# Optimization experiments

Measured on AMD Instinct MI355X. Metric: run time of the kernel, lower is better.

The kernel has to match this reference:

```python
import jax, jax.numpy as jnp
import numpy as np
import math

B, S, D, H, R, DFF = 4, 1024, 1024, 16, 64, 4096

def _layernorm(x, g, b, eps=1e-5):
    m = jnp.mean(x, axis=-1, keepdims=True)
    v = jnp.var(x, axis=-1, keepdims=True)
    return (x - m) / jnp.sqrt(v + eps) * g + b

def setup_inputs() -> dict:
    key = jax.random.key(0)
    ks = jax.random.split(key, 12)
    sc = 0.02
    return {
        "src": jax.random.normal(ks[0], (B, S, D), jnp.float32),
        "in_proj_w": jax.random.normal(ks[1], (3 * D, D), jnp.float32) * sc,
        "in_proj_b": jnp.zeros((3 * D,), jnp.float32),
        "out_proj_w": jax.random.normal(ks[2], (D, D), jnp.float32) * sc,
        "out_proj_b": jnp.zeros((D,), jnp.float32),
        "Qp_w": jax.random.normal(ks[3], (R, D), jnp.float32) * sc,
        "Qp_b": jnp.zeros((R,), jnp.float32),
        "Kp_w": jax.random.normal(ks[4], (R, D), jnp.float32) * sc,
        "Kp_b": jnp.zeros((R,), jnp.float32),
        "Vp_w": jax.random.normal(ks[5], (D, D), jnp.float32) * sc,
        "Vp_b": jnp.zeros((D,), jnp.float32),
        "lam": jnp.float32(0.5),
        "ff1_w": jax.random.normal(ks[6], (DFF, D), jnp.float32) * sc,
        "ff1_b": jnp.zeros((DFF,), jnp.float32),
        "ff2_w": jax.random.normal(ks[7], (D, DFF), jnp.float32) * sc,
        "ff2_b": jnp.zeros((D,), jnp.float32),
        "ln1_g": jnp.ones((D,), jnp.float32),
        "ln1_b": jnp.zeros((D,), jnp.float32),
        "ln2_g": jnp.ones((D,), jnp.float32),
        "ln2_b": jnp.zeros((D,), jnp.float32),
    }

def reference(src, in_proj_w, in_proj_b, out_proj_w, out_proj_b,
              Qp_w, Qp_b, Kp_w, Kp_b, Vp_w, Vp_b, lam,
              ff1_w, ff1_b, ff2_w, ff2_b, ln1_g, ln1_b, ln2_g, ln2_b):
    b, s, d = src.shape
    dh = d // H
    # ---- dense multi-head attention (torch nn.MultiheadAttention, eval) ----
    qkv = src @ in_proj_w.T + in_proj_b            # [B,S,3D]
    q, k, v = jnp.split(qkv, 3, axis=-1)
    q = q.reshape(b, s, H, dh).transpose(0, 2, 1, 3)  # [B,H,S,dh]
    k = k.reshape(b, s, H, dh).transpose(0, 2, 1, 3)
    v = v.reshape(b, s, H, dh).transpose(0, 2, 1, 3)
    scores = jnp.einsum('bhqd,bhkd->bhqk', q, k) / math.sqrt(dh)
    attn = jax.nn.softmax(scores, axis=-1)
    ctx = jnp.einsum('bhqk,bhkd->bhqd', attn, v)
    ctx = ctx.transpose(0, 2, 1, 3).reshape(b, s, d)
    dense_output = ctx @ out_proj_w.T + out_proj_b
    # ---- low-rank top-k sparse attention ----
    Q = src @ Qp_w.T + Qp_b                        # [B,S,R]
    K = src @ Kp_w.T + Kp_b
    V = src @ Vp_w.T + Vp_b                        # [B,S,D]
    QK = jnp.einsum('bqr,bkr->bqk', Q, K) / math.sqrt(R)
    aw = jax.nn.softmax(QK, axis=-1)               # [B,S,S]
    kk = max(1, int(s * 0.2))
    topv, topi = jax.lax.top_k(aw, kk)             # [B,S,kk]
    bi = jnp.arange(b)[:, None, None]
    si = jnp.arange(s)[None, :, None]
    sparse_attn = jnp.zeros_like(aw).at[bi, si, topi].set(topv)
    sparse_attn = sparse_attn / (jnp.sum(sparse_attn, axis=-1, keepdims=True) + 1e-9)
    sparse_output = jnp.einsum('bqk,bkd->bqd', sparse_attn, V)
    # ---- fuse, residual, norm, FFN ----
    sig = jax.nn.sigmoid(lam)
    fused = sig * dense_output + (1.0 - sig) * sparse_output
    x = _layernorm(src + fused, ln1_g, ln1_b)
    ff = jax.nn.relu(x @ ff1_w.T + ff1_b) @ ff2_w.T + ff2_b
    return _layernorm(x + ff, ln2_g, ln2_b)
```

## Files before the change

kernel.cpp:

```cpp
#include <hip/hip_runtime.h>
#include <hip/hip_bf16.h>
#include <math.h>

typedef __hip_bfloat16 bf16;
typedef __attribute__((ext_vector_type(8))) short short8;
typedef __attribute__((ext_vector_type(4))) float f32x4;

#define NB 4
#define NS 1024
#define ND 1024
#define NH 16
#define NDH 64
#define NR 64
#define NDFF 4096
#define NM (NB*NS)
#define NTOPK 204

static __device__ __forceinline__ float b2f(bf16 x) { return __bfloat162float(x); }
static __device__ __forceinline__ bf16  f2b(float x) { return __float2bfloat16(x); }
static __device__ __forceinline__ unsigned short bfbits(float x) {
  bf16 h = __float2bfloat16(x);
  return *reinterpret_cast<unsigned short*>(&h);
}

static __device__ __forceinline__ void gload_lds16(const void* g, void* l) {
  __builtin_amdgcn_global_load_lds(
      (const __attribute__((address_space(1))) void*)g,
      (__attribute__((address_space(3))) void*)l, 16, 0, 0);
}

template<int N> static __device__ __forceinline__ void vm_wait() {
  if constexpr (N == 0)       asm volatile("s_waitcnt vmcnt(0)" ::: "memory");
  else if constexpr (N == 2)  asm volatile("s_waitcnt vmcnt(2)" ::: "memory");
  else if constexpr (N == 4)  asm volatile("s_waitcnt vmcnt(4)" ::: "memory");
  else if constexpr (N == 6)  asm volatile("s_waitcnt vmcnt(6)" ::: "memory");
  else if constexpr (N == 8)  asm volatile("s_waitcnt vmcnt(8)" ::: "memory");
  else if constexpr (N == 12) asm volatile("s_waitcnt vmcnt(12)" ::: "memory");
  else static_assert(N == 0, "unsupported vmcnt");
}
static __device__ __forceinline__ void bar() {
  asm volatile("s_barrier" ::: "memory");
}

static __device__ __forceinline__ void ld8(const bf16* p, float* d) {
  const uint4 u = *(const uint4*)p;
  d[0] = __uint_as_float((u.x & 0xffffu) << 16);
  d[1] = __uint_as_float(u.x & 0xffff0000u);
  d[2] = __uint_as_float((u.y & 0xffffu) << 16);
  d[3] = __uint_as_float(u.y & 0xffff0000u);
  d[4] = __uint_as_float((u.z & 0xffffu) << 16);
  d[5] = __uint_as_float(u.z & 0xffff0000u);
  d[6] = __uint_as_float((u.w & 0xffffu) << 16);
  d[7] = __uint_as_float(u.w & 0xffff0000u);
}

static __device__ __forceinline__ float block_sum_256(float v, float* rbuf, int tid) {
  rbuf[tid] = v;
  __syncthreads();
  #pragma unroll
  for (int st = 128; st > 0; st >>= 1) {
    if (tid < st) rbuf[tid] += rbuf[tid + st];
    __syncthreads();
  }
  const float r = rbuf[0];
  __syncthreads();
  return r;
}

struct CastArgs {
  const float* in[6];
  bf16* out[6];
  unsigned end[6];
};
__global__ __launch_bounds__(256) void cast6_kernel(CastArgs a) {
  const unsigned b = blockIdx.x;
  int r = 0; unsigned base = 0;
  #pragma unroll
  for (int k = 0; k < 5; ++k)
    if (b >= a.end[k]) { r = k + 1; base = a.end[k]; }
  const float* in = a.in[r];
  bf16* out = a.out[r];
  const unsigned i = ((b - base) * 256 + threadIdx.x) * 4;
  const float4 v = *(const float4*)(in + i);
  uint2 o;
  o.x = (unsigned)bfbits(v.x) | ((unsigned)bfbits(v.y) << 16);
  o.y = (unsigned)bfbits(v.z) | ((unsigned)bfbits(v.w) << 16);
  *(uint2*)(out + i) = o;
}

__global__ __launch_bounds__(256) void pack_qk_kernel(
    const float* __restrict__ Qw, const float* __restrict__ Kw,
    const float* __restrict__ Qb, const float* __restrict__ Kb,
    bf16* __restrict__ w, float* __restrict__ bias) {
  const int r = blockIdx.x;
  const float* srcw = (r < 64) ? (Qw + (size_t)r * ND) : (Kw + (size_t)(r - 64) * ND);
  for (int i = threadIdx.x; i < ND; i += 256) w[(size_t)r * ND + i] = f2b(srcw[i]);
  if (r == 0)
    for (int i = threadIdx.x; i < 128; i += 256)
      bias[i] = (i < 64) ? Qb[i] : Kb[i - 64];
}

template<int BM, int BN, int BK, int BIAS, int RELU, int OUTF32>
__global__ __launch_bounds__(256) void mfma_gemm(
    const bf16* __restrict__ A, const bf16* __restrict__ W,
    const float* __restrict__ bias, void* __restrict__ C,
    int K, int lda, int ldb, int ldc,
    long long aHi, long long aLo, long long bHi, long long bLo,
    long long cHi, long long cLo, float scale)
{
  constexpr int WTM = BM / 2;
  constexpr int WTN = BN / 2;
  constexpr int AM = WTM / 16;
  constexpr int AN = WTN / 16;
  constexpr int KK = BK / 32;
  constexpr int SLOTS = BK / 8;
  constexpr int RPC = 512 / BK;
  constexpr int LPW = (BM * BK) / 2048 + (BN * BK) / 2048;
  __shared__ short As[2][BM * BK];
  __shared__ short Bs[2][BN * BK];
  const int tid  = threadIdx.x;
  const int lane = tid & 63;
  const int w    = tid >> 6;
  const int z    = blockIdx.z;
  const long long aOff = (long long)(z >> 4) * aHi + (long long)(z & 15) * aLo;
  const long long bOff = (long long)(z >> 4) * bHi + (long long)(z & 15) * bLo;
  const long long cOff = (long long)(z >> 4) * cHi + (long long)(z & 15) * cLo;

  int bx = blockIdx.x, by = blockIdx.y;
  if ((gridDim.x & 7) == 0) {
    const unsigned lin = blockIdx.y * gridDim.x + blockIdx.x;
    const unsigned Wd = gridDim.x >> 3;
    const unsigned xcd = lin & 7, i = lin >> 3;
    bx = (int)(xcd * Wd + (i % Wd));
    by = (int)(i / Wd);
  }
  const int m0 = by * BM;
  const int n0 = bx * BN;
  const int wr = w >> 1, wc = w & 1;
  const int lm = lane & 15, quad = lane >> 4;

  f32x4 acc[AM][AN];
  #pragma unroll
  for (int i = 0; i < AM; ++i)
    #pragma unroll
    for (int j = 0; j < AN; ++j) acc[i][j] = (f32x4){0.f, 0.f, 0.f, 0.f};

  const int slot = lane & (SLOTS - 1);
  const int sr   = lane / SLOTS;
  const int swz  = (BK == 32) ? ((sr >> 1) & 3) : (sr & 7);
  const int scol = (slot ^ swz) << 3;
  const int xv   = (BK == 32) ? ((lm >> 1) & 3) : (lm & 7);
  const bf16* Ab = A + aOff;
  const bf16* Bb = W + bOff;

  auto stage = [&](int buf, int k0) {
    #pragma unroll
    for (int t = 0; t < (BM * BK) / 2048; ++t) {
      const int row = w * (BM / 4) + t * RPC;
      gload_lds16(Ab + (long long)(m0 + row + sr) * lda + k0 + scol, &As[buf][row * BK]);
    }
    #pragma unroll
    for (int t = 0; t < (BN * BK) / 2048; ++t) {
      const int row = w * (BN / 4) + t * RPC;
      gload_lds16(Bb + (long long)(n0 + row + sr) * ldb + k0 + scol, &Bs[buf][row * BK]);
    }
  };
  auto compute = [&](int buf) {
    #pragma unroll
    for (int kk = 0; kk < KK; ++kk) {
      const int cb = ((kk * 4 + quad) ^ xv) << 3;
      short8 af[AM], bfr[AN];
      #pragma unroll
      for (int i = 0; i < AM; ++i)
        af[i] = *(const short8*)&As[buf][(wr * WTM + i * 16 + lm) * BK + cb];
      #pragma unroll
      for (int j = 0; j < AN; ++j)
        bfr[j] = *(const short8*)&Bs[buf][(wc * WTN + j * 16 + lm) * BK + cb];
      #pragma unroll
      for (int i = 0; i < AM; ++i)
        #pragma unroll
        for (int j = 0; j < AN; ++j)
          acc[i][j] = __builtin_amdgcn_mfma_f32_16x16x32_bf16(af[i], bfr[j], acc[i][j], 0, 0, 0);
    }
  };

  stage(0, 0);
  int cur = 0;
  for (int k0 = BK; k0 < K; k0 += BK) {
    stage(cur ^ 1, k0);
    vm_wait<LPW>();
    bar();
    compute(cur);
    bar();
    cur ^= 1;
  }
  vm_wait<0>();
  bar();
  compute(cur);

  #pragma unroll
  for (int i = 0; i < AM; ++i) {
    #pragma unroll
    for (int j = 0; j < AN; ++j) {
      const int n = n0 + wc * WTN + j * 16 + lm;
      const float bj = BIAS ? bias[n] : 0.f;
      #pragma unroll
      for (int rr = 0; rr < 4; ++rr) {
        const int m = m0 + wr * WTM + i * 16 + quad * 4 + rr;
        float v = acc[i][j][rr] * scale + bj;
        if (RELU) v = fmaxf(v, 0.f);
        const long long co = cOff + (long long)m * ldc + n;
        if (OUTF32) ((float*)C)[co] = v;
        else        ((bf16*)C)[co] = f2b(v);
      }
    }
  }
}

__global__ __launch_bounds__(256) void attn_kernel(
    const bf16* __restrict__ qkv,
    const bf16* __restrict__ Vt,
    bf16* __restrict__ ctx)
{
  __shared__ short smem[2][2][64 * 64];
  const int tid = threadIdx.x, lane = tid & 63, w = tid >> 6;
  const int lm = lane & 15, quad = lane >> 4;
  const int z = blockIdx.y, b = z >> 4, h = z & 15;
  const int q0 = blockIdx.x * 128;
  const bf16* Qb = qkv + (long long)b * NS * 3072 + h * 64;
  const bf16* Kb = Qb + ND;
  const bf16* Vb = Vt + (long long)z * (NDH * NS);

  short8 qf[2][2];
  #pragma unroll
  for (int j = 0; j < 2; ++j)
    #pragma unroll
    for (int kk = 0; kk < 2; ++kk)
      qf[j][kk] = *(const short8*)(Qb + (long long)(q0 + w * 32 + j * 16 + lm) * 3072
                                      + kk * 32 + quad * 8);

  const int slot = lane & 7, sr = lane >> 3;
  const int scol = (slot ^ sr) << 3;

  auto stage = [&](int buf, int t) {
    #pragma unroll
    for (int u = 0; u < 2; ++u) {
      const int row = w * 16 + u * 8;
      gload_lds16(Kb + (long long)(t * 64 + row + sr) * 3072 + scol,
                  &smem[buf][0][row * 64]);
    }
    #pragma unroll
    for (int u = 0; u < 2; ++u) {
      const int row = w * 16 + u * 8;
      gload_lds16(Vb + (long long)(row + sr) * NS + t * 64 + scol,
                  &smem[buf][1][row * 64]);
    }
  };

  f32x4 o[4][2];
  #pragma unroll
  for (int i = 0; i < 4; ++i)
    #pragma unroll
    for (int j = 0; j < 2; ++j) o[i][j] = (f32x4){0.f, 0.f, 0.f, 0.f};
  float m[2] = {-1e30f, -1e30f}, l[2] = {0.f, 0.f};

  stage(0, 0);
  for (int t = 0; t < 16; ++t) {
    const int buf = t & 1;
    if (t < 15) { stage(buf ^ 1, t + 1); vm_wait<4>(); }
    else        { vm_wait<0>(); }
    bar();

    f32x4 st[4][2];
    #pragma unroll
    for (int i = 0; i < 4; ++i)
      #pragma unroll
      for (int j = 0; j < 2; ++j) st[i][j] = (f32x4){0.f, 0.f, 0.f, 0.f};
    #pragma unroll
    for (int kk = 0; kk < 2; ++kk) {
      const int cb = ((kk * 4 + quad) ^ (lm & 7)) << 3;
      short8 ka[4];
      #pragma unroll
      for (int i = 0; i < 4; ++i)
        ka[i] = *(const short8*)&smem[buf][0][(i * 16 + lm) * 64 + cb];
      #pragma unroll
      for (int i = 0; i < 4; ++i)
        #pragma unroll
        for (int j = 0; j < 2; ++j)
          st[i][j] = __builtin_amdgcn_mfma_f32_16x16x32_bf16(ka[i], qf[j][kk], st[i][j], 0, 0, 0);
    }

    #pragma unroll
    for (int j = 0; j < 2; ++j) {
      float pm = -1e30f;
      #pragma unroll
      for (int i = 0; i < 4; ++i)
        #pragma unroll
        for (int r = 0; r < 4; ++r) {
          st[i][j][r] *= 0.125f;
          pm = fmaxf(pm, st[i][j][r]);
        }
      pm = fmaxf(pm, __shfl_xor(pm, 16, 64));
      pm = fmaxf(pm, __shfl_xor(pm, 32, 64));
      const float mn = fmaxf(m[j], pm);
      const float sc = __expf(m[j] - mn);
      float ps = 0.f;
      #pragma unroll
      for (int i = 0; i < 4; ++i)
        #pragma unroll
        for (int r = 0; r < 4; ++r) {
          const float e = __expf(st[i][j][r] - mn);
          st[i][j][r] = e;
          ps += e;
        }
      ps += __shfl_xor(ps, 16, 64);
      ps += __shfl_xor(ps, 32, 64);
      l[j] = l[j] * sc + ps;
      m[j] = mn;
      #pragma unroll
      for (int i = 0; i < 4; ++i)
        #pragma unroll
        for (int r = 0; r < 4; ++r) o[i][j][r] *= sc;
    }

    unsigned u0[4][2], u1[4][2];
    #pragma unroll
    for (int i = 0; i < 4; ++i)
      #pragma unroll
      for (int j = 0; j < 2; ++j) {
        u0[i][j] = (unsigned)bfbits(st[i][j][0]) | ((unsigned)bfbits(st[i][j][1]) << 16);
        u1[i][j] = (unsigned)bfbits(st[i][j][2]) | ((unsigned)bfbits(st[i][j][3]) << 16);
      }
    const int s0l = ((quad & 1) * 2) * 16 + lm;
    const int s1l = s0l + 16;
    const bool hi = (quad >> 1) != 0;

    #pragma unroll
    for (int kk = 0; kk < 2; ++kk) {
      short8 pf[2];
      #pragma unroll
      for (int j = 0; j < 2; ++j) {
        const unsigned a0 = __shfl(u0[kk * 2][j],     s0l, 64);
        const unsigned a1 = __shfl(u1[kk * 2][j],     s0l, 64);
        const unsigned b0 = __shfl(u0[kk * 2 + 1][j], s0l, 64);
        const unsigned b1 = __shfl(u1[kk * 2 + 1][j], s0l, 64);
        const unsigned c0 = __shfl(u0[kk * 2][j],     s1l, 64);
        const unsigned c1 = __shfl(u1[kk * 2][j],     s1l, 64);
        const unsigned d0 = __shfl(u0[kk * 2 + 1][j], s1l, 64);
        const unsigned d1 = __shfl(u1[kk * 2 + 1][j], s1l, 64);
        union { uint4 u; short8 s; } cv;
        cv.u.x = hi ? b0 : a0; cv.u.y = hi ? b1 : a1;
        cv.u.z = hi ? d0 : c0; cv.u.w = hi ? d1 : c1;
        pf[j] = cv.s;
      }
      const int cb = ((kk * 4 + quad) ^ (lm & 7)) << 3;
      short8 va[4];
      #pragma unroll
      for (int i = 0; i < 4; ++i)
        va[i] = *(const short8*)&smem[buf][1][(i * 16 + lm) * 64 + cb];
      #pragma unroll
      for (int i = 0; i < 4; ++i)
        #pragma unroll
        for (int j = 0; j < 2; ++j)
          o[i][j] = __builtin_amdgcn_mfma_f32_16x16x32_bf16(va[i], pf[j], o[i][j], 0, 0, 0);
    }
    bar();
  }

  short (*OL)[72] = (short(*)[72])&smem[0][0][0];
  #pragma unroll
  for (int j = 0; j < 2; ++j) {
    const float inv = 1.f / l[j];
    #pragma unroll
    for (int i = 0; i < 4; ++i) {
      uint2 u;
      u.x = (unsigned)bfbits(o[i][j][0] * inv) | ((unsigned)bfbits(o[i][j][1] * inv) << 16);
      u.y = (unsigned)bfbits(o[i][j][2] * inv) | ((unsigned)bfbits(o[i][j][3] * inv) << 16);
      *(uint2*)&OL[w * 32 + j * 16 + lm][i * 16 + quad * 4] = u;
    }
  }
  __syncthreads();
  {
    const int q = tid >> 1, c = (tid & 1) * 32;
    const uint4 r0 = *(const uint4*)&OL[q][c];
    const uint4 r1 = *(const uint4*)&OL[q][c + 8];
    const uint4 r2 = *(const uint4*)&OL[q][c + 16];
    const uint4 r3 = *(const uint4*)&OL[q][c + 24];
    bf16* dst = ctx + ((long long)(b * NS + q0 + q)) * 1024 + h * 64 + c;
    ((uint4*)dst)[0] = r0; ((uint4*)dst)[1] = r1;
    ((uint4*)dst)[2] = r2; ((uint4*)dst)[3] = r3;
  }
}

__global__ __launch_bounds__(256) void transpose_v_kernel(
    const bf16* __restrict__ qkv, bf16* __restrict__ Vt) {
  __shared__ short T[64][72];
  const int tid = threadIdx.x;
  const int h = blockIdx.y;
  const int b = blockIdx.z;
  const int s0 = blockIdx.x * 64;
  const bf16* src = qkv + ((long long)b * NS + s0) * 3072 + 2 * ND + h * 64;
  {
    const int s = tid >> 2, c = (tid & 3) * 16;
    const uint4 a0 = *(const uint4*)(src + (long long)s * 3072 + c);
    const uint4 a1 = *(const uint4*)(src + (long long)s * 3072 + c + 8);
    *(uint4*)&T[s][c] = a0; *(uint4*)&T[s][c + 8] = a1;
  }
  __syncthreads();
  {
    const int d = tid >> 2, c = (tid & 3) * 16;
    unsigned wds[8];
    #pragma unroll
    for (int u = 0; u < 8; ++u) {
      const unsigned lo = (unsigned short)T[c + 2 * u][d];
      const unsigned hi = (unsigned short)T[c + 2 * u + 1][d];
      wds[u] = lo | (hi << 16);
    }
    bf16* dst = Vt + (long long)(b * NH + h) * (NDH * NS) + (long long)d * NS + s0 + c;
    uint4 o0, o1;
    o0.x = wds[0]; o0.y = wds[1]; o0.z = wds[2]; o0.w = wds[3];
    o1.x = wds[4]; o1.y = wds[5]; o1.z = wds[6]; o1.w = wds[7];
    ((uint4*)dst)[0] = o0; ((uint4*)dst)[1] = o1;
  }
}

__global__ __launch_bounds__(256) void transpose_sq_kernel(
    const bf16* __restrict__ src, bf16* __restrict__ dst) {
  __shared__ short T[64][72];
  const int tid = threadIdx.x;
  const int b = blockIdx.z;
  const int s0 = blockIdx.x * 64, d0 = blockIdx.y * 64;
  const bf16* sp = src + ((long long)b * NS + s0) * ND + d0;
  {
    const int s = tid >> 2, c = (tid & 3) * 16;
    const uint4 a0 = *(const uint4*)(sp + (long long)s * ND + c);
    const uint4 a1 = *(const uint4*)(sp + (long long)s * ND + c + 8);
    *(uint4*)&T[s][c] = a0; *(uint4*)&T[s][c + 8] = a1;
  }
  __syncthreads();
  {
    const int d = tid >> 2, c = (tid & 3) * 16;
    unsigned wds[8];
    #pragma unroll
    for (int u = 0; u < 8; ++u) {
      const unsigned lo = (unsigned short)T[c + 2 * u][d];
      const unsigned hi = (unsigned short)T[c + 2 * u + 1][d];
      wds[u] = lo | (hi << 16);
    }
    bf16* dp = dst + ((long long)b * ND + d0 + d) * NS + s0 + c;
    uint4 o0, o1;
    o0.x = wds[0]; o0.y = wds[1]; o0.z = wds[2]; o0.w = wds[3];
    o1.x = wds[4]; o1.y = wds[5]; o1.z = wds[6]; o1.w = wds[7];
    ((uint4*)dp)[0] = o0; ((uint4*)dp)[1] = o1;
  }
}

__global__ __launch_bounds__(256) void sparse_select_kernel(
    const float* __restrict__ S, bf16* __restrict__ aw)
{
  __shared__ unsigned hist[4][256];
  const int tid = threadIdx.x;
  const int lane = tid & 63;
  const int wv = tid >> 6;
  const long long row = (long long)blockIdx.x * 4 + wv;

  float sv[16];
  const float* sp = S + row * 1024 + lane * 16;
  #pragma unroll
  for (int c = 0; c < 4; ++c) {
    const float4 v = ((const float4*)sp)[c];
    sv[4*c] = v.x; sv[4*c+1] = v.y; sv[4*c+2] = v.z; sv[4*c+3] = v.w;
  }
  unsigned key[16];
  #pragma unroll
  for (int j = 0; j < 16; ++j) {
    const unsigned u = __float_as_uint(sv[j]);
    key[j] = (u & 0x80000000u) ? ~u : (u | 0x80000000u);
  }

  unsigned pref = 0u;
  int need = NTOPK;
  #pragma unroll
  for (int p = 3; p >= 0; --p) {
    *(uint4*)&hist[wv][lane * 4] = (uint4){0u, 0u, 0u, 0u};
    __syncthreads();
    const int sh = (p + 1) * 8;
    #pragma unroll
    for (int j = 0; j < 16; ++j) {
      const bool part = (p == 3) || ((key[j] >> sh) == pref);
      if (part) atomicAdd(&hist[wv][(key[j] >> (p * 8)) & 255u], 1u);
    }
    __syncthreads();
    const unsigned h0 = hist[wv][4*lane],     h1 = hist[wv][4*lane + 1];
    const unsigned h2 = hist[wv][4*lane + 2], h3 = hist[wv][4*lane + 3];
    const unsigned s3 = h3, s2 = h2 + s3, s1 = h1 + s2, s0 = h0 + s1;
    unsigned sum = s0;
    #pragma unroll
    for (int d2 = 1; d2 < 64; d2 <<= 1) {
      const unsigned t = __shfl_down(sum, d2, 64);
      if (lane < 64 - d2) sum += t;
    }
    const unsigned above = sum - s0;
    const unsigned cum[4]  = {above + s0, above + s1, above + s2, above + s3};
    const unsigned next[4] = {above + s1, above + s2, above + s3, above};
    unsigned candPref = 0u; int candNeed = 0; bool has = false;
    #pragma unroll
    for (int i = 0; i < 4; ++i) {
      if ((int)cum[i] >= need && (int)next[i] < need) {
        has = true;
        candPref = (pref << 8) | (unsigned)(4 * lane + i);
        candNeed = need - (int)next[i];
      }
    }
    const unsigned long long m = __ballot(has);
    const int srcLane = (int)(__ffsll((long long)m) - 1);
    pref = (unsigned)__shfl((int)candPref, srcLane, 64);
    need = __shfl(candNeed, srcLane, 64);
  }

  const unsigned T = pref;
  const unsigned tb = (T & 0x80000000u) ? (T ^ 0x80000000u) : ~T;
  const float thr = __uint_as_float(tb);

  float wvv[16];
  float psTop = 0.f, psAll = 0.f;
  #pragma unroll
  for (int j = 0; j < 16; ++j) {
    const float e = __expf(sv[j] - thr);
    psAll += e;
    const float wt = (key[j] >= T) ? e : 0.f;
    psTop += wt;
    wvv[j] = wt;
  }
  #pragma unroll
  for (int s = 1; s < 64; s <<= 1) {
    psTop += __shfl_xor(psTop, s, 64);
    psAll += __shfl_xor(psAll, s, 64);
  }
  const float inv = 1.f / (psTop + 1e-9f * psAll);

  uint4 o0, o1;
  o0.x = (unsigned)bfbits(wvv[0]*inv)  | ((unsigned)bfbits(wvv[1]*inv)  << 16);
  o0.y = (unsigned)bfbits(wvv[2]*inv)  | ((unsigned)bfbits(wvv[3]*inv)  << 16);
  o0.z = (unsigned)bfbits(wvv[4]*inv)  | ((unsigned)bfbits(wvv[5]*inv)  << 16);
  o0.w = (unsigned)bfbits(wvv[6]*inv)  | ((unsigned)bfbits(wvv[7]*inv)  << 16);
  o1.x = (unsigned)bfbits(wvv[8]*inv)  | ((unsigned)bfbits(wvv[9]*inv)  << 16);
  o1.y = (unsigned)bfbits(wvv[10]*inv) | ((unsigned)bfbits(wvv[11]*inv) << 16);
  o1.z = (unsigned)bfbits(wvv[12]*inv) | ((unsigned)bfbits(wvv[13]*inv) << 16);
  o1.w = (unsigned)bfbits(wvv[14]*inv) | ((unsigned)bfbits(wvv[15]*inv) << 16);
  bf16* op = aw + row * 1024 + lane * 16;
  ((uint4*)op)[0] = o0; ((uint4*)op)[1] = o1;
}

__global__ __launch_bounds__(256) void fuse_ln1_kernel(
    const float* __restrict__ src, const bf16* __restrict__ dense,
    const bf16* __restrict__ sparse, const float* __restrict__ lam,
    const float* __restrict__ g, const float* __restrict__ beta,
    bf16* __restrict__ x1)
{
  __shared__ float y[ND];
  __shared__ float rbuf[256];
  const int tid = threadIdx.x;
  const size_t base = (size_t)blockIdx.x * ND;
  const float sig = 1.f / (1.f + __expf(-lam[0]));
  const float c1 = 1.f - sig;
  float s1 = 0.f, s2 = 0.f;
  #pragma unroll
  for (int j = 0; j < 4; ++j) {
    const int i = tid + (j << 8);
    const float v = src[base + i] + sig * b2f(dense[base + i]) + c1 * b2f(sparse[base + i]);
    y[i] = v; s1 += v; s2 += v * v;
  }
  const float sum1 = block_sum_256(s1, rbuf, tid);
  const float sum2 = block_sum_256(s2, rbuf, tid);
  const float mean = sum1 * (1.f / ND);
  const float var  = sum2 * (1.f / ND) - mean * mean;
  const float rstd = rsqrtf(var + 1e-5f);
  #pragma unroll
  for (int j = 0; j < 4; ++j) {
    const int i = tid + (j << 8);
    x1[base + i] = f2b((y[i] - mean) * rstd * g[i] + beta[i]);
  }
}

__global__ __launch_bounds__(256) void ln2_kernel(
    const bf16* __restrict__ x1, const bf16* __restrict__ ff,
    const float* __restrict__ g, const float* __restrict__ beta,
    float* __restrict__ outp)
{
  __shared__ float y[ND];
  __shared__ float rbuf[256];
  const int tid = threadIdx.x;
  const size_t base = (size_t)blockIdx.x * ND;
  float s1 = 0.f, s2 = 0.f;
  #pragma unroll
  for (int j = 0; j < 4; ++j) {
    const int i = tid + (j << 8);
    const float v = b2f(x1[base + i]) + b2f(ff[base + i]);
    y[i] = v; s1 += v; s2 += v * v;
  }
  const float sum1 = block_sum_256(s1, rbuf, tid);
  const float sum2 = block_sum_256(s2, rbuf, tid);
  const float mean = sum1 * (1.f / ND);
  const float var  = sum2 * (1.f / ND) - mean * mean;
  const float rstd = rsqrtf(var + 1e-5f);
  #pragma unroll
  for (int j = 0; j < 4; ++j) {
    const int i = tid + (j << 8);
    outp[base + i] = (y[i] - mean) * rstd * g[i] + beta[i];
  }
}

extern "C" void kernel_launch(void* const* d_in, const int* in_sizes, int n_in,
                              void* d_out, int out_size, void* d_ws, size_t ws_size,
                              hipStream_t stream)
{
  const float* src        = (const float*)d_in[0];
  const float* in_proj_w  = (const float*)d_in[1];
  const float* in_proj_b  = (const float*)d_in[2];
  const float* out_proj_w = (const float*)d_in[3];
  const float* out_proj_b = (const float*)d_in[4];
  const float* Qp_w  = (const float*)d_in[5];
  const float* Qp_b  = (const float*)d_in[6];
  const float* Kp_w  = (const float*)d_in[7];
  const float* Kp_b  = (const float*)d_in[8];
  const float* Vp_w  = (const float*)d_in[9];
  const float* Vp_b  = (const float*)d_in[10];
  const float* lam   = (const float*)d_in[11];
  const float* ff1_w = (const float*)d_in[12];
  const float* ff1_b = (const float*)d_in[13];
  const float* ff2_w = (const float*)d_in[14];
  const float* ff2_b = (const float*)d_in[15];
  const float* ln1_g = (const float*)d_in[16];
  const float* ln1_b = (const float*)d_in[17];
  const float* ln2_g = (const float*)d_in[18];
  const float* ln2_b = (const float*)d_in[19];
  (void)in_sizes; (void)n_in; (void)out_size; (void)ws_size;

  char* ws = (char*)d_ws;
  size_t off = 0;
  auto take = [&](size_t bytes) -> void* {
    void* p = ws + off; off += (bytes + 255) & ~(size_t)255; return p;
  };
  bf16*  src_bf  = (bf16*) take((size_t)NM * ND * 2);
  bf16*  w_qkv   = (bf16*) take((size_t)3 * ND * ND * 2);
  bf16*  w_out   = (bf16*) take((size_t)ND * ND * 2);
  bf16*  w_vp    = (bf16*) take((size_t)ND * ND * 2);
  bf16*  w_ff1   = (bf16*) take((size_t)NDFF * ND * 2);
  bf16*  w_ff2   = (bf16*) take((size_t)ND * NDFF * 2);
  bf16*  w_qk    = (bf16*) take((size_t)128 * ND * 2);
  float* bias_qk = (float*)take(128 * 4);
  const size_t mark = off;
  bf16*  qkv     = (bf16*) take((size_t)NM * 3 * ND * 2);
  bf16*  Vt_all  = (bf16*) take((size_t)NH * NS * NS * 2);
  bf16*  Vt_old  = (bf16*) take((size_t)NH * NDH * NS * 2);
  bf16*  ctx     = (bf16*) take((size_t)NM * ND * 2);
  bf16*  dense   = (bf16*) take((size_t)NM * ND * 2);
  bf16*  QKs_bf  = (bf16*) take((size_t)NM * 128 * 2);
  bf16*  Vsp     = (bf16*) take((size_t)NM * ND * 2);
  bf16*  sparse  = (bf16*) take((size_t)NM * ND * 2);
  (void)Vt_old;
  bf16*  x1    = (bf16*)(ws + mark);
  bf16*  h1    = (bf16*)(ws + mark + (size_t)NM * ND * 2);
  bf16*  ffout = (bf16*)(ws + mark + (size_t)NM * ND * 2 + (size_t)NM * NDFF * 2);
  bf16*  aw    = (bf16*)(ws + mark + 2 * (size_t)NM * ND * 2 + (size_t)NM * NDFF * 2);
  float* S_sp  = (float*)(ws + mark + (size_t)NM * ND * 2);
  bf16*  Vsp_t = (bf16*)ctx;

  const dim3 blk(256);
  {
    CastArgs a;
    a.in[0] = src;        a.out[0] = src_bf;
    a.in[1] = in_proj_w;  a.out[1] = w_qkv;
    a.in[2] = out_proj_w; a.out[2] = w_out;
    a.in[3] = Vp_w;       a.out[3] = w_vp;
    a.in[4] = ff1_w;      a.out[4] = w_ff1;
    a.in[5] = ff2_w;      a.out[5] = w_ff2;
    a.end[0] = 4096; a.end[1] = 7168; a.end[2] = 8192;
    a.end[3] = 9216; a.end[4] = 13312; a.end[5] = 17408;
    cast6_kernel<<<dim3(17408), blk, 0, stream>>>(a);
  }
  pack_qk_kernel<<<dim3(128), blk, 0, stream>>>(Qp_w, Kp_w, Qp_b, Kp_b, w_qk, bias_qk);

  mfma_gemm<128,128,32,1,0,0><<<dim3(3*ND/128, NM/128, 1), blk, 0, stream>>>(
      src_bf, w_qkv, in_proj_b, qkv, ND, ND, ND, 3*ND, 0,0, 0,0, 0,0, 1.f);

  transpose_v_kernel<<<dim3(NS/64, NH, NB), blk, 0, stream>>>(qkv, Vt_all);
  attn_kernel<<<dim3(NS/128, NB*NH), blk, 0, stream>>>(qkv, Vt_all, ctx);

  mfma_gemm<128,64,64,1,0,0><<<dim3(ND/64, NM/128, 1), blk, 0, stream>>>(
      ctx, w_out, out_proj_b, dense, ND, ND, ND, ND, 0,0, 0,0, 0,0, 1.f);
  mfma_gemm<128,64,64,1,0,0><<<dim3(2, NM/128, 1), blk, 0, stream>>>(
      src_bf, w_qk, bias_qk, QKs_bf, ND, ND, ND, 128, 0,0, 0,0, 0,0, 1.f);
  mfma_gemm<128,64,64,0,0,1><<<dim3(NS/64, NS/128, NB), blk, 0, stream>>>(
      QKs_bf, QKs_bf + 64, nullptr, S_sp, 64, 128, 128, NS,
      0, (long long)NS*128, 0, (long long)NS*128, 0, (long long)NS*NS, 0.125f);
  mfma_gemm<128,64,64,1,0,0><<<dim3(ND/64, NM/128, 1), blk, 0, stream>>>(
      src_bf, w_vp, Vp_b, Vsp, ND, ND, ND, ND, 0,0, 0,0, 0,0, 1.f);
  transpose_sq_kernel<<<dim3(NS/64, ND/64, NB), blk, 0, stream>>>(Vsp, Vsp_t);
  sparse_select_kernel<<<dim3(NM/4), blk, 0, stream>>>(S_sp, aw);
  mfma_gemm<128,64,64,0,0,0><<<dim3(ND/64, NS/128, NB), blk, 0, stream>>>(
      aw, Vsp_t, nullptr, sparse, NS, NS, NS, ND,
      0, (long long)NS*ND, 0, (long long)ND*NS, 0, (long long)NS*ND, 1.f);
  fuse_ln1_kernel<<<dim3(NM), blk, 0, stream>>>(src, dense, sparse, lam, ln1_g, ln1_b, x1);
  mfma_gemm<128,128,32,1,1,0><<<dim3(NDFF/128, NM/128, 1), blk, 0, stream>>>(
      x1, w_ff1, ff1_b, h1, ND, ND, ND, NDFF, 0,0, 0,0, 0,0, 1.f);
  mfma_gemm<128,64,64,1,0,0><<<dim3(ND/64, NM/128, 1), blk, 0, stream>>>(
      h1, w_ff2, ff2_b, ffout, NDFF, NDFF, NDFF, ND, 0,0, 0,0, 0,0, 1.f);
  ln2_kernel<<<dim3(NM), blk, 0, stream>>>(x1, ffout, ln2_g, ln2_b, (float*)d_out);
}
```

Measured before the change: 445.9 us.

## Load GEMM B operand directly into registers instead of staging through LDS

The GEMM kernel no longer stages the weight (B) tile in shared memory. Each lane loads its MFMA B fragments straight from global memory into double-buffered registers, with the loop unrolled by two so the register buffer index stays compile-time. This cuts LDS traffic and footprint, which may allow more blocks per CU. In exchange there are more global loads without cross-wave reuse, higher register pressure, and a different vmcnt accounting that must match the number of loads issued.

```diff
diff --git a/kernel.cpp b/kernel.cpp
--- a/kernel.cpp
+++ b/kernel.cpp
@@ -1,6 +1,7 @@
 #include <hip/hip_runtime.h>
 #include <hip/hip_bf16.h>
 #include <math.h>
+#include <type_traits>
 
 typedef __hip_bfloat16 bf16;
 typedef __attribute__((ext_vector_type(8))) short short8;
@@ -31,11 +32,9 @@
 
 template<int N> static __device__ __forceinline__ void vm_wait() {
   if constexpr (N == 0)       asm volatile("s_waitcnt vmcnt(0)" ::: "memory");
-  else if constexpr (N == 2)  asm volatile("s_waitcnt vmcnt(2)" ::: "memory");
   else if constexpr (N == 4)  asm volatile("s_waitcnt vmcnt(4)" ::: "memory");
   else if constexpr (N == 6)  asm volatile("s_waitcnt vmcnt(6)" ::: "memory");
   else if constexpr (N == 8)  asm volatile("s_waitcnt vmcnt(8)" ::: "memory");
-  else if constexpr (N == 12) asm volatile("s_waitcnt vmcnt(12)" ::: "memory");
   else static_assert(N == 0, "unsupported vmcnt");
 }
 static __device__ __forceinline__ void bar() {
@@ -115,9 +114,9 @@
   constexpr int KK = BK / 32;
   constexpr int SLOTS = BK / 8;
   constexpr int RPC = 512 / BK;
-  constexpr int LPW = (BM * BK) / 2048 + (BN * BK) / 2048;
+  constexpr int ASTG = (BM * BK) / 2048;
+  constexpr int LPW  = ASTG + AN * KK;
   __shared__ short As[2][BM * BK];
-  __shared__ short Bs[2][BN * BK];
   const int tid  = threadIdx.x;
   const int lane = tid & 63;
   const int w    = tid >> 6;
@@ -151,52 +150,64 @@
   const int scol = (slot ^ swz) << 3;
   const int xv   = (BK == 32) ? ((lm >> 1) & 3) : (lm & 7);
   const bf16* Ab = A + aOff;
-  const bf16* Bb = W + bOff;
-
-  auto stage = [&](int buf, int k0) {
-    #pragma unroll
-    for (int t = 0; t < (BM * BK) / 2048; ++t) {
-      const int row = w * (BM / 4) + t * RPC;
+  const bf16* Bb = W + bOff + (long long)(n0 + wc * WTN + lm) * ldb + quad * 8;
+
+  auto stageA = [&](int buf, int t) {
+    const int k0 = t * BK;
+    #pragma unroll
+    for (int u = 0; u < ASTG; ++u) {
+      const int row = w * (BM / 4) + u * RPC;
       gload_lds16(Ab + (long long)(m0 + row + sr) * lda + k0 + scol, &As[buf][row * BK]);
     }
-    #pragma unroll
-    for (int t = 0; t < (BN * BK) / 2048; ++t) {
-      const int row = w * (BN / 4) + t * RPC;
-      gload_lds16(Bb + (long long)(n0 + row + sr) * ldb + k0 + scol, &Bs[buf][row * BK]);
-    }
   };
-  auto compute = [&](int buf) {
+
+  short8 brg[2][AN * KK];
+  auto loadB = [&](auto BUF, int t) {
+    constexpr int bu = decltype(BUF)::value;
+    const int k0 = t * BK;
+    #pragma unroll
+    for (int j = 0; j < AN; ++j)
+      #pragma unroll
+      for (int kk = 0; kk < KK; ++kk)
+        brg[bu][j * KK + kk] =
+            *(const short8*)(Bb + (long long)(j * 16) * ldb + k0 + kk * 32);
+  };
+
+  auto compute = [&](auto BUF) {
+    constexpr int bu = decltype(BUF)::value;
     #pragma unroll
     for (int kk = 0; kk < KK; ++kk) {
       const int cb = ((kk * 4 + quad) ^ xv) << 3;
-      short8 af[AM], bfr[AN];
+      short8 af[AM];
       #pragma unroll
       for (int i = 0; i < AM; ++i)
-        af[i] = *(const short8*)&As[buf][(wr * WTM + i * 16 + lm) * BK + cb];
-      #pragma unroll
-      for (int j = 0; j < AN; ++j)
-        bfr[j] = *(const short8*)&Bs[buf][(wc * WTN + j * 16 + lm) * BK + cb];
+        af[i] = *(const short8*)&As[bu][(wr * WTM + i * 16 + lm) * BK + cb];
       #pragma unroll
       for (int i = 0; i < AM; ++i)
         #pragma unroll
         for (int j = 0; j < AN; ++j)
-          acc[i][j] = __builtin_amdgcn_mfma_f32_16x16x32_bf16(af[i], bfr[j], acc[i][j], 0, 0, 0);
+          acc[i][j] = __builtin_amdgcn_mfma_f32_16x16x32_bf16(
+              af[i], brg[bu][j * KK + kk], acc[i][j], 0, 0, 0);
     }
   };
-
-  stage(0, 0);
-  int cur = 0;
-  for (int k0 = BK; k0 < K; k0 += BK) {
-    stage(cur ^ 1, k0);
-    vm_wait<LPW>();
-    bar();
-    compute(cur);
-    bar();
-    cur ^= 1;
-  }
-  vm_wait<0>();
-  bar();
-  compute(cur);
+  const std::integral_constant<int, 0> B0{};
+  const std::integral_constant<int, 1> B1{};
+
+  const int nt = K / BK;
+  stageA(0, 0); loadB(B0, 0);
+  if (nt == 1) {
+    vm_wait<0>(); bar(); compute(B0);
+  } else {
+    for (int t = 1; t + 1 < nt; t += 2) {
+      stageA(1, t);     loadB(B1, t);
+      vm_wait<LPW>(); bar(); compute(B0); bar();
+      stageA(0, t + 1); loadB(B0, t + 1);
+      vm_wait<LPW>(); bar(); compute(B1); bar();
+    }
+    stageA(1, nt - 1); loadB(B1, nt - 1);
+    vm_wait<LPW>(); bar(); compute(B0); bar();
+    vm_wait<0>(); bar(); compute(B1);
+  }
 
   #pragma unroll
   for (int i = 0; i < AM; ++i) {
```

Result: slower. 544.4 us (+22.1%).
